# Performance work log

Measured on AMD Instinct MI355X. Metric: run time of the kernel, lower is better.

The kernel has to match this reference:

```python
import jax, jax.numpy as jnp
import numpy as np

AFWD = 0.999
EPS = 1e-05


def setup_inputs() -> dict:
    key = jax.random.key(0)
    N, L = 8192, 4096
    x = jax.random.normal(key, (N, L), dtype=jnp.float32)
    m = jnp.zeros((L,), dtype=jnp.float32)    # EMA mean buffer (init 0)
    var = jnp.ones((L,), dtype=jnp.float32)   # EMA var buffer (init 1)
    return {"x": x, "m": m, "var": var}


def reference(x, m, var):
    """Online-normalization forward: sequential scan over the N (row) dim,
    vectorized over the L feature dim. Matches ControlNormalization.forward."""
    afwd = AFWD

    def step(carry, xt):
        mu, v = carry                      # each [L]
        scale = jnp.sqrt(v + EPS)
        d = xt - mu
        out = d / scale
        v_new = afwd * v + afwd * (1.0 - afwd) * d * d
        mu_new = mu + (1.0 - afwd) * d
        return (mu_new, v_new), out

    _, out = jax.lax.scan(step, (m, var), x)  # out: [N, L]
    return out
```

## Files before the change

kernel.cpp:

```cpp
#include <hip/hip_runtime.h>
#include <math.h>

#define AFWD 0.999f
#define ONE_MINUS_A (1.0f - 0.999f)
#define KCOEF (0.999f * (1.0f - 0.999f))
#define EPSV 1e-5f

typedef float floatx4 __attribute__((ext_vector_type(4)));

__global__ __launch_bounds__(256) void
passA(const float* __restrict__ x, float* __restrict__ Bmu,
      float* __restrict__ See, float* __restrict__ Te, int L4, int CH) {
  int idx  = blockIdx.x * blockDim.x + threadIdx.x;
  int col4 = idx % L4;
  int c    = idx / L4;
  const floatx4* xv = (const floatx4*)x;
  int base = c * CH * L4 + col4;

  float mu[4] = {0.f, 0.f, 0.f, 0.f};
  float s[4]  = {0.f, 0.f, 0.f, 0.f};
  float t[4]  = {0.f, 0.f, 0.f, 0.f};

#pragma unroll 4
  for (int i = 0; i < CH; ++i) {
    floatx4 v = xv[base + i * L4];
#pragma unroll
    for (int k = 0; k < 4; ++k) {
      float e = v[k] - mu[k];
      s[k] = fmaf(AFWD, s[k], e * e);
      t[k] += e;
      mu[k] = fmaf(ONE_MINUS_A, e, mu[k]);
    }
  }

  int o = c * L4 + col4;
  floatx4 om = {mu[0], mu[1], mu[2], mu[3]};
  floatx4 os = {s[0], s[1], s[2], s[3]};
  floatx4 ot = {t[0], t[1], t[2], t[3]};
  ((floatx4*)Bmu)[o] = om;
  ((floatx4*)See)[o] = os;
  ((floatx4*)Te)[o]  = ot;
}

__device__ __forceinline__ float
weighted_scan_incl(float u, float A, int c, int C, float* sm) {
  float p = u;
  float w = A;
  for (int off = 1; off < C; off <<= 1) {
    __syncthreads();
    sm[c] = p;
    __syncthreads();
    if (c >= off) p = fmaf(w, sm[c - off], p);
    w *= w;
  }
  return p;
}

__global__ void
passB_scan(const float* __restrict__ m, const float* __restrict__ var,
           const float* __restrict__ Bmu, const float* __restrict__ See,
           const float* __restrict__ Te, float* __restrict__ Ms,
           float* __restrict__ Vs, int L, int C, float A, float c_eg,
           float Sgg) {
  extern __shared__ float sm[];
  int l = blockIdx.x;
  int c = threadIdx.x;
  int o = c * L + l;

  float bmu = Bmu[o];
  float see = See[o];
  float te  = Te[o];
  float M0 = m[l];
  float V0 = var[l];

  float Ac = 1.0f, Ap = A;
#pragma unroll
  for (int b = 0; b < 10; ++b) {
    if (c & (1 << b)) Ac *= Ap;
    Ap *= Ap;
  }

  float p = weighted_scan_incl(bmu, A, c, C, sm);
  __syncthreads();
  sm[c] = p;
  __syncthreads();
  float M = fmaf(Ac, M0, (c > 0) ? sm[c - 1] : 0.0f);

  float w = KCOEF * fmaf(M * M, Sgg, fmaf(-2.0f * c_eg * M, te, see));
  float q = weighted_scan_incl(w, A, c, C, sm);
  __syncthreads();
  sm[c] = q;
  __syncthreads();
  float V = fmaf(Ac, V0, (c > 0) ? sm[c - 1] : 0.0f);

  Ms[o] = M;
  Vs[o] = V;
}

__global__ __launch_bounds__(256) void
passC(const float* __restrict__ x, const float* __restrict__ Ms,
      const float* __restrict__ Vs, float* __restrict__ out, int L4, int CH) {
  int idx  = blockIdx.x * blockDim.x + threadIdx.x;
  int col4 = idx % L4;
  int c    = idx / L4;
  const floatx4* xv = (const floatx4*)x;
  floatx4* ov = (floatx4*)out;
  int base = c * CH * L4 + col4;

  int o = c * L4 + col4;
  floatx4 m4 = ((const floatx4*)Ms)[o];
  floatx4 v4 = ((const floatx4*)Vs)[o];
  float mu[4] = {m4[0], m4[1], m4[2], m4[3]};
  float vv[4] = {v4[0], v4[1], v4[2], v4[3]};

#pragma unroll 4
  for (int i = 0; i < CH; ++i) {
    floatx4 v = xv[base + i * L4];
    floatx4 oe;
#pragma unroll
    for (int k = 0; k < 4; ++k) {
      float d = v[k] - mu[k];
      oe[k] = d * rsqrtf(vv[k] + EPSV);
      vv[k] = fmaf(AFWD, vv[k], KCOEF * (d * d));
      mu[k] = fmaf(ONE_MINUS_A, d, mu[k]);
    }
    __builtin_nontemporal_store(oe, &ov[base + i * L4]);
  }
}

extern "C" void kernel_launch(void* const* d_in, const int* in_sizes, int n_in,
                              void* d_out, int out_size, void* d_ws, size_t ws_size,
                              hipStream_t stream) {
  const float* x   = (const float*)d_in[0];
  const float* m   = (const float*)d_in[1];
  const float* var = (const float*)d_in[2];
  float* out = (float*)d_out;

  int L  = in_sizes[1];
  int N  = in_sizes[0] / L;
  int L4 = L / 4;

  int C = 128;
  while (C > 1 && ((size_t)5 * C * L * sizeof(float) > ws_size || (N % C) != 0))
    C >>= 1;
  int CH = N / C;

  double a = 0.999;
  float A    = (float)pow(a, (double)CH);
  float c_eg = (float)pow(a, (double)(CH - 1));
  float Sgg  = (float)(pow(a, (double)(CH - 1)) * (1.0 - pow(a, (double)CH)) / (1.0 - a));

  float* ws  = (float*)d_ws;
  size_t CL  = (size_t)C * L;
  float* Bmu = ws;
  float* See = ws + CL;
  float* Te  = ws + 2 * CL;
  float* Ms  = ws + 3 * CL;
  float* Vs  = ws + 4 * CL;

  int threadsBig = C * L4;
  passA<<<threadsBig / 256, 256, 0, stream>>>(x, Bmu, See, Te, L4, CH);
  passB_scan<<<L, C, C * sizeof(float), stream>>>(m, var, Bmu, See, Te, Ms, Vs,
                                                  L, C, A, c_eg, Sgg);
  passC<<<threadsBig / 256, 256, 0, stream>>>(x, Ms, Vs, out, L4, CH);
}
```

Measured before the change: 92.43 us.

## Fuse chunk-carry scan into output pass with per-thread serial prefix

```diff
diff --git a/kernel.cpp b/kernel.cpp
--- a/kernel.cpp
+++ b/kernel.cpp
@@ -7,6 +7,7 @@
 #define EPSV 1e-5f
 
 typedef float floatx4 __attribute__((ext_vector_type(4)));
+
 
 __global__ __launch_bounds__(256) void
 passA(const float* __restrict__ x, float* __restrict__ Bmu,
@@ -20,7 +21,6 @@
   float mu[4] = {0.f, 0.f, 0.f, 0.f};
   float s[4]  = {0.f, 0.f, 0.f, 0.f};
   float t[4]  = {0.f, 0.f, 0.f, 0.f};
-
 #pragma unroll 4
   for (int i = 0; i < CH; ++i) {
     floatx4 v = xv[base + i * L4];
@@ -32,7 +32,6 @@
       mu[k] = fmaf(ONE_MINUS_A, e, mu[k]);
     }
   }
-
   int o = c * L4 + col4;
   floatx4 om = {mu[0], mu[1], mu[2], mu[3]};
   floatx4 os = {s[0], s[1], s[2], s[3]};
@@ -42,76 +41,43 @@
   ((floatx4*)Te)[o]  = ot;
 }
 
-__device__ __forceinline__ float
-weighted_scan_incl(float u, float A, int c, int C, float* sm) {
-  float p = u;
-  float w = A;
-  for (int off = 1; off < C; off <<= 1) {
-    __syncthreads();
-    sm[c] = p;
-    __syncthreads();
-    if (c >= off) p = fmaf(w, sm[c - off], p);
-    w *= w;
-  }
-  return p;
-}
-
-__global__ void
-passB_scan(const float* __restrict__ m, const float* __restrict__ var,
-           const float* __restrict__ Bmu, const float* __restrict__ See,
-           const float* __restrict__ Te, float* __restrict__ Ms,
-           float* __restrict__ Vs, int L, int C, float A, float c_eg,
-           float Sgg) {
-  extern __shared__ float sm[];
-  int l = blockIdx.x;
-  int c = threadIdx.x;
-  int o = c * L + l;
-
-  float bmu = Bmu[o];
-  float see = See[o];
-  float te  = Te[o];
-  float M0 = m[l];
-  float V0 = var[l];
-
-  float Ac = 1.0f, Ap = A;
-#pragma unroll
-  for (int b = 0; b < 10; ++b) {
-    if (c & (1 << b)) Ac *= Ap;
-    Ap *= Ap;
-  }
-
-  float p = weighted_scan_incl(bmu, A, c, C, sm);
-  __syncthreads();
-  sm[c] = p;
-  __syncthreads();
-  float M = fmaf(Ac, M0, (c > 0) ? sm[c - 1] : 0.0f);
-
-  float w = KCOEF * fmaf(M * M, Sgg, fmaf(-2.0f * c_eg * M, te, see));
-  float q = weighted_scan_incl(w, A, c, C, sm);
-  __syncthreads();
-  sm[c] = q;
-  __syncthreads();
-  float V = fmaf(Ac, V0, (c > 0) ? sm[c - 1] : 0.0f);
-
-  Ms[o] = M;
-  Vs[o] = V;
-}
-
 __global__ __launch_bounds__(256) void
-passC(const float* __restrict__ x, const float* __restrict__ Ms,
-      const float* __restrict__ Vs, float* __restrict__ out, int L4, int CH) {
+passWC(const float* __restrict__ x, const float* __restrict__ m,
+       const float* __restrict__ var, const float* __restrict__ Bmu,
+       const float* __restrict__ See, const float* __restrict__ Te,
+       float* __restrict__ out, int L4, int CH,
+       float A, float c_eg, float Sgg) {
   int idx  = blockIdx.x * blockDim.x + threadIdx.x;
   int col4 = idx % L4;
   int c    = idx / L4;
-  const floatx4* xv = (const floatx4*)x;
+  const floatx4* xv   = (const floatx4*)x;
+  const floatx4* bmu4 = (const floatx4*)Bmu;
+  const floatx4* see4 = (const floatx4*)See;
+  const floatx4* te4  = (const floatx4*)Te;
   floatx4* ov = (floatx4*)out;
   int base = c * CH * L4 + col4;
 
-  int o = c * L4 + col4;
-  floatx4 m4 = ((const floatx4*)Ms)[o];
-  floatx4 v4 = ((const floatx4*)Vs)[o];
-  float mu[4] = {m4[0], m4[1], m4[2], m4[3]};
-  float vv[4] = {v4[0], v4[1], v4[2], v4[3]};
+  float M[4], V[4];
+  {
+    floatx4 m4 = ((const floatx4*)m)[col4];
+    floatx4 v4 = ((const floatx4*)var)[col4];
+#pragma unroll
+    for (int k = 0; k < 4; ++k) { M[k] = m4[k]; V[k] = v4[k]; }
+  }
+#pragma unroll 4
+  for (int cc = 0; cc < c; ++cc) {
+    int o = cc * L4 + col4;
+    floatx4 bb = bmu4[o];
+    floatx4 ss = see4[o];
+    floatx4 tt = te4[o];
+#pragma unroll
+    for (int k = 0; k < 4; ++k) {
+      float sum = fmaf(M[k] * M[k], Sgg,
+                       fmaf(-2.0f * c_eg * M[k], tt[k], ss[k]));
+      V[k] = fmaf(A, V[k], KCOEF * sum);
+      M[k] = fmaf(A, M[k], bb[k]);
+    }
+  }
 
 #pragma unroll 4
   for (int i = 0; i < CH; ++i) {
@@ -119,10 +85,10 @@
     floatx4 oe;
 #pragma unroll
     for (int k = 0; k < 4; ++k) {
-      float d = v[k] - mu[k];
-      oe[k] = d * rsqrtf(vv[k] + EPSV);
-      vv[k] = fmaf(AFWD, vv[k], KCOEF * (d * d));
-      mu[k] = fmaf(ONE_MINUS_A, d, mu[k]);
+      float d = v[k] - M[k];
+      oe[k] = d * rsqrtf(V[k] + EPSV);
+      V[k] = fmaf(AFWD, V[k], KCOEF * (d * d));
+      M[k] = fmaf(ONE_MINUS_A, d, M[k]);
     }
     __builtin_nontemporal_store(oe, &ov[base + i * L4]);
   }
@@ -141,7 +107,8 @@
   int L4 = L / 4;
 
   int C = 128;
-  while (C > 1 && ((size_t)5 * C * L * sizeof(float) > ws_size || (N % C) != 0))
+  while (C > 1 &&
+         ((size_t)3 * C * L * sizeof(float) > ws_size || (N % C) != 0))
     C >>= 1;
   int CH = N / C;
 
@@ -155,12 +122,9 @@
   float* Bmu = ws;
   float* See = ws + CL;
   float* Te  = ws + 2 * CL;
-  float* Ms  = ws + 3 * CL;
-  float* Vs  = ws + 4 * CL;
 
-  int threadsBig = C * L4;
-  passA<<<threadsBig / 256, 256, 0, stream>>>(x, Bmu, See, Te, L4, CH);
-  passB_scan<<<L, C, C * sizeof(float), stream>>>(m, var, Bmu, See, Te, Ms, Vs,
-                                                  L, C, A, c_eg, Sgg);
-  passC<<<threadsBig / 256, 256, 0, stream>>>(x, Ms, Vs, out, L4, CH);
+  int gridBlocks = (C * L4) / 256;
+  passA<<<gridBlocks, 256, 0, stream>>>(x, Bmu, See, Te, L4, CH);
+  passWC<<<gridBlocks, 256, 0, stream>>>(x, m, var, Bmu, See, Te, out, L4, CH,
+                                         A, c_eg, Sgg);
 }
```

New measurement: 85.27 us. 7.7% less time.
